# Kernel tuning notes

Hardware: AMD Instinct MI355X
Metric: run time of the kernel (lower is better)

Reference implementation:

```python
import jax, jax.numpy as jnp
import numpy as np

WIN = 3  # win_size from init


def setup_inputs() -> dict:
    key = jax.random.key(0)
    ks = jax.random.split(key, 7)
    B, H, W, d = 8, 128, 128, 128
    N = H * W
    s = d ** -0.5  # param init scale
    return {
        "x": jax.random.normal(ks[0], (B, N, d), dtype=jnp.float32),
        "Wq": jax.random.normal(ks[1], (d, d), dtype=jnp.float32) * s,
        "bq": jax.random.normal(ks[2], (d,), dtype=jnp.float32) * 0.01,
        "Wk": jax.random.normal(ks[3], (d, d), dtype=jnp.float32) * s,
        "bk": jax.random.normal(ks[4], (d,), dtype=jnp.float32) * 0.01,
        "Wv": jax.random.normal(ks[5], (d, d), dtype=jnp.float32) * s,
        "bv": jax.random.normal(ks[6], (d,), dtype=jnp.float32) * 0.01,
        "H": H,
        "W": W,
    }


def reference(x, Wq, bq, Wk, bk, Wv, bv, H, W):
    B, N, d = x.shape
    scale = d ** -0.5
    pad = WIN // 2

    q = (x @ Wq + bq).reshape(B, H, W, d)
    k = (x @ Wk + bk).reshape(B, H, W, d)
    v = (x @ Wv + bv).reshape(B, H, W, d)

    # zero-pad spatial dims (matches F.pad); padded neighbors get logit 0, not -inf
    k_pad = jnp.pad(k, ((0, 0), (pad, pad), (pad, pad), (0, 0)))
    v_pad = jnp.pad(v, ((0, 0), (pad, pad), (pad, pad), (0, 0)))

    scores_l, vs_l = [], []
    for dy in range(WIN):
        for dx in range(WIN):
            k_slice = k_pad[:, dy:dy + H, dx:dx + W]   # [B,H,W,d]
            v_slice = v_pad[:, dy:dy + H, dx:dx + W]
            scores_l.append(jnp.einsum("bhwd,bhwd->bhw", q, k_slice) * scale)
            vs_l.append(v_slice)

    scores = jnp.stack(scores_l, axis=-1)            # [B,H,W,9]
    prob = jax.nn.softmax(scores, axis=-1)           # [B,H,W,9]
    v_stk = jnp.stack(vs_l, axis=-1)                 # [B,H,W,d,9]
    out = jnp.einsum("bhwn,bhwdn->bhwd", prob, v_stk)
    return out.reshape(B, N, d)
```

## Files before the change

kernel.cpp:

```cpp
#include <hip/hip_runtime.h>
#include <stdint.h>

#define B_ 8
#define H_ 128
#define W_ 128
#define D_ 128
#define N_ (H_*W_)
#define M_ (B_*N_)

typedef __attribute__((ext_vector_type(8))) short short8;
typedef __attribute__((ext_vector_type(4))) float floatx4;

typedef const __attribute__((address_space(1))) void* gas_t;
typedef __attribute__((address_space(3))) void* las_t;

__device__ inline unsigned short f2bf(float f){
  union { float f; unsigned int i; } c; c.f = f;
  unsigned int x = c.i;
  x += 0x7FFF + ((x >> 16) & 1);
  return (unsigned short)(x >> 16);
}
__device__ inline float bflo(unsigned int u){
  union { unsigned int i; float f; } c; c.i = u << 16; return c.f;
}
__device__ inline float bfhi(unsigned int u){
  union { unsigned int i; float f; } c; c.i = u & 0xFFFF0000u; return c.f;
}

__global__ void wtrans_kernel(const float* __restrict__ Wq, const float* __restrict__ Wk,
                              const float* __restrict__ Wv, unsigned short* __restrict__ Wt){
  const float* src = blockIdx.x == 0 ? Wq : (blockIdx.x == 1 ? Wk : Wv);
  unsigned short* dst = Wt + blockIdx.x * (D_*D_);
  const int i = blockIdx.y * 256 + threadIdx.x;
  const int k = i >> 7, n = i & 127;
  dst[n*D_ + k] = f2bf(src[i]);
}

__global__ __launch_bounds__(256, 2) void qkv_gemm_kernel(
    const float* __restrict__ x, const unsigned short* __restrict__ Wt,
    const float* __restrict__ bq, const float* __restrict__ bk, const float* __restrict__ bv,
    unsigned short* __restrict__ Q, unsigned short* __restrict__ K, unsigned short* __restrict__ V)
{
  const int rowTile = blockIdx.x;

  __shared__ unsigned short lds[32768];

  const int t = threadIdx.x;
  const int wave = t >> 6, lane = t & 63;

  {
    const float* xrow = x + (size_t)rowTile * 128 * D_;
    #pragma unroll
    for (int p = 0; p < 8; ++p){
      int s = p*256 + t;
      int r = s >> 4, cp = s & 15, c = cp ^ (r & 7);
      const float* gp = xrow + r*D_ + c*8;
      float4 f0 = *(const float4*)gp;
      float4 f1 = *(const float4*)(gp + 4);
      uint4 pk;
      pk.x = (unsigned)f2bf(f0.x) | ((unsigned)f2bf(f0.y) << 16);
      pk.y = (unsigned)f2bf(f0.z) | ((unsigned)f2bf(f0.w) << 16);
      pk.z = (unsigned)f2bf(f1.x) | ((unsigned)f2bf(f1.y) << 16);
      pk.w = (unsigned)f2bf(f1.z) | ((unsigned)f2bf(f1.w) << 16);
      *(uint4*)&lds[s*8] = pk;
    }
  }

  const int wm = (wave >> 1) * 64, wn = (wave & 1) * 64;
  const int m0 = lane & 15, quad = lane >> 4;

  #pragma unroll
  for (int which = 0; which < 3; ++which){
    const float* bias = which == 0 ? bq : (which == 1 ? bk : bv);
    unsigned short* Out = which == 0 ? Q : (which == 1 ? K : V);
    const unsigned short* Wsel = Wt + which * (D_*D_);

    #pragma unroll
    for (int p = 0; p < 8; ++p){
      int s = p*256 + t;
      int n = s >> 4, cp = s & 15, c = cp ^ (n & 7);
      const unsigned short* gp = Wsel + n*128 + c*8;
      unsigned short* lp = (unsigned short*)lds + 16384 + p*2048 + wave*512;
      __builtin_amdgcn_global_load_lds((gas_t)(const void*)gp, (las_t)(void*)lp, 16, 0, 0);
    }
    __syncthreads();

    floatx4 acc[4][4] = {};
    #pragma unroll
    for (int kk = 0; kk < 4; ++kk){
      short8 a[4], b[4];
      #pragma unroll
      for (int i = 0; i < 4; ++i){
        int row = wm + i*16 + m0;
        int c = (kk*4 + quad) ^ (row & 7);
        a[i] = *(const short8*)&lds[row*128 + c*8];
      }
      #pragma unroll
      for (int j = 0; j < 4; ++j){
        int n = wn + j*16 + m0;
        int c = (kk*4 + quad) ^ (n & 7);
        b[j] = *(const short8*)&lds[16384 + n*128 + c*8];
      }
      #pragma unroll
      for (int i = 0; i < 4; ++i)
        #pragma unroll
        for (int j = 0; j < 4; ++j)
          acc[i][j] = __builtin_amdgcn_mfma_f32_16x16x32_bf16(a[i], b[j], acc[i][j], 0, 0, 0);
    }

    __syncthreads();
    unsigned short* Outp = Out + (size_t)rowTile * 128 * D_;
    #pragma unroll
    for (int half = 0; half < 2; ++half){
      if ((wave >> 1) == half){
        #pragma unroll
        for (int j = 0; j < 4; ++j){
          const int col = wn + j*16 + m0;
          const float bb = bias[col];
          #pragma unroll
          for (int i = 0; i < 4; ++i){
            #pragma unroll
            for (int r = 0; r < 4; ++r){
              int lrow = i*16 + quad*4 + r;
              lds[16384 + lrow*136 + col] = f2bf(acc[i][j][r] + bb);
            }
          }
        }
      }
      __syncthreads();
      #pragma unroll
      for (int p = 0; p < 4; ++p){
        int rr = p*16 + (t >> 4), cc = t & 15;
        uint4 vv = *(const uint4*)&lds[16384 + rr*136 + cc*8];
        *(uint4*)(Outp + half*8192 + p*2048 + t*8) = vv;
      }
      __syncthreads();
    }
  }
}

__global__ __launch_bounds__(256, 4) void attn_kernel(
    const unsigned short* __restrict__ Q, const unsigned short* __restrict__ K,
    const unsigned short* __restrict__ V, float* __restrict__ out)
{
  const int t = threadIdx.x;
  const int e16 = t & 15;
  const int pix = blockIdx.x * 16 + (t >> 4);
  const int w = pix & 127;
  const int h = (pix >> 7) & 127;
  const int bbase = pix & ~(N_ - 1);
  const float scale = 0.08838834764831845f;
  const int doff = e16 * 8;
  const size_t off = (size_t)pix * D_ + doff;

  int npix[9]; bool okm[9];
  #pragma unroll
  for (int i = 0; i < 9; ++i){
    const int dy = i/3 - 1, dx = i%3 - 1;
    const int hh = h + dy, ww = w + dx;
    okm[i] = ((unsigned)hh < 128u) && ((unsigned)ww < 128u);
    const int hc = min(max(hh, 0), 127);
    const int wc = min(max(ww, 0), 127);
    npix[i] = bbase + hc*W_ + wc;
  }

  uint4 qu = *(const uint4*)(Q + off);
  uint4 ku[9];
  #pragma unroll
  for (int i = 0; i < 9; ++i)
    ku[i] = *(const uint4*)(K + (size_t)npix[i]*D_ + doff);

  float q[8];
  {
    unsigned uu[4] = {qu.x, qu.y, qu.z, qu.w};
    #pragma unroll
    for (int e = 0; e < 4; ++e){
      q[e*2]     = bflo(uu[e]) * scale;
      q[e*2 + 1] = bfhi(uu[e]) * scale;
    }
  }

  float s[9];
  #pragma unroll
  for (int i = 0; i < 9; ++i){
    unsigned uu[4] = {ku[i].x, ku[i].y, ku[i].z, ku[i].w};
    float acc = 0.f;
    #pragma unroll
    for (int e = 0; e < 4; ++e){
      acc += q[e*2]     * bflo(uu[e]);
      acc += q[e*2 + 1] * bfhi(uu[e]);
    }
    s[i] = okm[i] ? acc : 0.f;
  }

  uint4 vu[9];
  #pragma unroll
  for (int i = 0; i < 9; ++i)
    vu[i] = *(const uint4*)(V + (size_t)npix[i]*D_ + doff);

  #pragma unroll
  for (int i = 0; i < 9; ++i){
    s[i] += __shfl_xor(s[i], 1, 64);
    s[i] += __shfl_xor(s[i], 2, 64);
    s[i] += __shfl_xor(s[i], 4, 64);
    s[i] += __shfl_xor(s[i], 8, 64);
  }

  float m = s[0];
  #pragma unroll
  for (int i = 1; i < 9; ++i) m = fmaxf(m, s[i]);
  float l = 0.f;
  float p[9];
  #pragma unroll
  for (int i = 0; i < 9; ++i){ p[i] = __expf(s[i] - m); l += p[i]; }
  const float inv = 1.f / l;

  float o[8];
  #pragma unroll
  for (int d = 0; d < 8; ++d) o[d] = 0.f;
  #pragma unroll
  for (int i = 0; i < 9; ++i){
    const float pi = okm[i] ? p[i] * inv : 0.f;
    unsigned uu[4] = {vu[i].x, vu[i].y, vu[i].z, vu[i].w};
    #pragma unroll
    for (int e = 0; e < 4; ++e){
      o[e*2]     += pi * bflo(uu[e]);
      o[e*2 + 1] += pi * bfhi(uu[e]);
    }
  }

  float* op = out + off;
  *(float4*)op       = make_float4(o[0], o[1], o[2], o[3]);
  *(float4*)(op + 4) = make_float4(o[4], o[5], o[6], o[7]);
}

extern "C" void kernel_launch(void* const* d_in, const int* in_sizes, int n_in,
                              void* d_out, int out_size, void* d_ws, size_t ws_size,
                              hipStream_t stream)
{
  const float* x  = (const float*)d_in[0];
  const float* Wq = (const float*)d_in[1];
  const float* bq = (const float*)d_in[2];
  const float* Wk = (const float*)d_in[3];
  const float* bk = (const float*)d_in[4];
  const float* Wv = (const float*)d_in[5];
  const float* bv = (const float*)d_in[6];
  float* out = (float*)d_out;

  char* ws = (char*)d_ws;
  unsigned short* Wt = (unsigned short*)ws;
  unsigned short* Q  = (unsigned short*)(ws + (1<<17));
  unsigned short* K  = (unsigned short*)(ws + (1<<17) + (size_t)M_*D_*2);
  unsigned short* V  = (unsigned short*)(ws + (1<<17) + (size_t)2*M_*D_*2);

  hipLaunchKernelGGL(wtrans_kernel, dim3(3, 64), dim3(256), 0, stream, Wq, Wk, Wv, Wt);
  hipLaunchKernelGGL(qkv_gemm_kernel, dim3(M_/128), dim3(256), 0, stream,
                     x, Wt, bq, bk, bv, Q, K, V);
  hipLaunchKernelGGL(attn_kernel, dim3(M_/16), dim3(256), 0, stream, Q, K, V, out);
}
```

Baseline: 184.8 us.

## Retile QKV GEMM into 64-row by 32-column blocks with register-resident x fragments

The QKV projection GEMM now splits its output columns into four 32-wide groups across blockIdx.x and uses 64-row tiles, raising the block count and allowing 4 blocks per CU. Each wave loads its x fragment straight from global memory into MFMA registers, converts it to bf16 there, and skips the LDS staging of x. Only the 32-column weight slices for Q, K and V go through LDS. The epilogue no longer transposes through LDS: operands are swapped in the MFMA and each lane writes packed bf16 directly. In exchange, x is fetched by four blocks instead of one, which leans on cache reuse, and the output stores are narrower and less coalesced.

```diff
diff --git a/kernel.cpp b/kernel.cpp
--- a/kernel.cpp
+++ b/kernel.cpp
@@ -36,105 +36,78 @@
   dst[n*D_ + k] = f2bf(src[i]);
 }
 
-__global__ __launch_bounds__(256, 2) void qkv_gemm_kernel(
+__global__ __launch_bounds__(256, 4) void qkv_gemm_kernel(
     const float* __restrict__ x, const unsigned short* __restrict__ Wt,
     const float* __restrict__ bq, const float* __restrict__ bk, const float* __restrict__ bv,
     unsigned short* __restrict__ Q, unsigned short* __restrict__ K, unsigned short* __restrict__ V)
 {
-  const int rowTile = blockIdx.x;
-
-  __shared__ unsigned short lds[32768];
+  const int cg = blockIdx.x;
+  const int rowTile = blockIdx.y;
+
+  __shared__ unsigned short lds[12288];
 
   const int t = threadIdx.x;
   const int wave = t >> 6, lane = t & 63;
-
+  const int m0 = lane & 15, quad = lane >> 4;
+
+  #pragma unroll
+  for (int which = 0; which < 3; ++which){
+    const unsigned short* Wsel = Wt + which*(D_*D_) + cg*32*D_;
+    #pragma unroll
+    for (int p = 0; p < 2; ++p){
+      int s = p*256 + t;
+      int n = s >> 4, cp = s & 15, c = cp ^ (n & 7);
+      __builtin_amdgcn_global_load_lds((gas_t)(const void*)(Wsel + n*128 + c*8),
+          (las_t)(void*)((unsigned short*)lds + which*4096 + p*2048 + wave*512), 16, 0, 0);
+    }
+  }
+
+  short8 a[4];
   {
-    const float* xrow = x + (size_t)rowTile * 128 * D_;
-    #pragma unroll
-    for (int p = 0; p < 8; ++p){
-      int s = p*256 + t;
-      int r = s >> 4, cp = s & 15, c = cp ^ (r & 7);
-      const float* gp = xrow + r*D_ + c*8;
-      float4 f0 = *(const float4*)gp;
-      float4 f1 = *(const float4*)(gp + 4);
-      uint4 pk;
-      pk.x = (unsigned)f2bf(f0.x) | ((unsigned)f2bf(f0.y) << 16);
-      pk.y = (unsigned)f2bf(f0.z) | ((unsigned)f2bf(f0.w) << 16);
-      pk.z = (unsigned)f2bf(f1.x) | ((unsigned)f2bf(f1.y) << 16);
-      pk.w = (unsigned)f2bf(f1.z) | ((unsigned)f2bf(f1.w) << 16);
-      *(uint4*)&lds[s*8] = pk;
-    }
-  }
-
-  const int wm = (wave >> 1) * 64, wn = (wave & 1) * 64;
-  const int m0 = lane & 15, quad = lane >> 4;
-
+    const float* xrow = x + (size_t)(rowTile*64 + wave*16 + m0) * D_ + quad*8;
+    float4 f[4][2];
+    #pragma unroll
+    for (int kk = 0; kk < 4; ++kk){
+      f[kk][0] = *(const float4*)(xrow + kk*32);
+      f[kk][1] = *(const float4*)(xrow + kk*32 + 4);
+    }
+    __builtin_amdgcn_sched_barrier(0);
+    #pragma unroll
+    for (int kk = 0; kk < 4; ++kk){
+      short8 v;
+      v[0] = (short)f2bf(f[kk][0].x); v[1] = (short)f2bf(f[kk][0].y);
+      v[2] = (short)f2bf(f[kk][0].z); v[3] = (short)f2bf(f[kk][0].w);
+      v[4] = (short)f2bf(f[kk][1].x); v[5] = (short)f2bf(f[kk][1].y);
+      v[6] = (short)f2bf(f[kk][1].z); v[7] = (short)f2bf(f[kk][1].w);
+      a[kk] = v;
+    }
+  }
+  __syncthreads();
+
+  const int row = rowTile*64 + wave*16 + m0;
   #pragma unroll
   for (int which = 0; which < 3; ++which){
+    floatx4 acc[2] = {};
+    #pragma unroll
+    for (int kk = 0; kk < 4; ++kk){
+      #pragma unroll
+      for (int j = 0; j < 2; ++j){
+        int n = j*16 + m0;
+        int c = (kk*4 + quad) ^ (n & 7);
+        short8 b = *(const short8*)&lds[which*4096 + n*128 + c*8];
+        acc[j] = __builtin_amdgcn_mfma_f32_16x16x32_bf16(b, a[kk], acc[j], 0, 0, 0);
+      }
+    }
     const float* bias = which == 0 ? bq : (which == 1 ? bk : bv);
     unsigned short* Out = which == 0 ? Q : (which == 1 ? K : V);
-    const unsigned short* Wsel = Wt + which * (D_*D_);
-
-    #pragma unroll
-    for (int p = 0; p < 8; ++p){
-      int s = p*256 + t;
-      int n = s >> 4, cp = s & 15, c = cp ^ (n & 7);
-      const unsigned short* gp = Wsel + n*128 + c*8;
-      unsigned short* lp = (unsigned short*)lds + 16384 + p*2048 + wave*512;
-      __builtin_amdgcn_global_load_lds((gas_t)(const void*)gp, (las_t)(void*)lp, 16, 0, 0);
-    }
-    __syncthreads();
-
-    floatx4 acc[4][4] = {};
-    #pragma unroll
-    for (int kk = 0; kk < 4; ++kk){
-      short8 a[4], b[4];
-      #pragma unroll
-      for (int i = 0; i < 4; ++i){
-        int row = wm + i*16 + m0;
-        int c = (kk*4 + quad) ^ (row & 7);
-        a[i] = *(const short8*)&lds[row*128 + c*8];
-      }
-      #pragma unroll
-      for (int j = 0; j < 4; ++j){
-        int n = wn + j*16 + m0;
-        int c = (kk*4 + quad) ^ (n & 7);
-        b[j] = *(const short8*)&lds[16384 + n*128 + c*8];
-      }
-      #pragma unroll
-      for (int i = 0; i < 4; ++i)
-        #pragma unroll
-        for (int j = 0; j < 4; ++j)
-          acc[i][j] = __builtin_amdgcn_mfma_f32_16x16x32_bf16(a[i], b[j], acc[i][j], 0, 0, 0);
-    }
-
-    __syncthreads();
-    unsigned short* Outp = Out + (size_t)rowTile * 128 * D_;
-    #pragma unroll
-    for (int half = 0; half < 2; ++half){
-      if ((wave >> 1) == half){
-        #pragma unroll
-        for (int j = 0; j < 4; ++j){
-          const int col = wn + j*16 + m0;
-          const float bb = bias[col];
-          #pragma unroll
-          for (int i = 0; i < 4; ++i){
-            #pragma unroll
-            for (int r = 0; r < 4; ++r){
-              int lrow = i*16 + quad*4 + r;
-              lds[16384 + lrow*136 + col] = f2bf(acc[i][j][r] + bb);
-            }
-          }
-        }
-      }
-      __syncthreads();
-      #pragma unroll
-      for (int p = 0; p < 4; ++p){
-        int rr = p*16 + (t >> 4), cc = t & 15;
-        uint4 vv = *(const uint4*)&lds[16384 + rr*136 + cc*8];
-        *(uint4*)(Outp + half*8192 + p*2048 + t*8) = vv;
-      }
-      __syncthreads();
+    #pragma unroll
+    for (int j = 0; j < 2; ++j){
+      const int col = cg*32 + j*16 + quad*4;
+      const float4 bb = *(const float4*)&bias[col];
+      uint2 pk;
+      pk.x = (unsigned)f2bf(acc[j][0] + bb.x) | ((unsigned)f2bf(acc[j][1] + bb.y) << 16);
+      pk.y = (unsigned)f2bf(acc[j][2] + bb.z) | ((unsigned)f2bf(acc[j][3] + bb.w) << 16);
+      *(uint2*)(Out + (size_t)row * D_ + col) = pk;
     }
   }
 }
@@ -254,7 +227,7 @@
   unsigned short* V  = (unsigned short*)(ws + (1<<17) + (size_t)2*M_*D_*2);
 
   hipLaunchKernelGGL(wtrans_kernel, dim3(3, 64), dim3(256), 0, stream, Wq, Wk, Wv, Wt);
-  hipLaunchKernelGGL(qkv_gemm_kernel, dim3(M_/128), dim3(256), 0, stream,
+  hipLaunchKernelGGL(qkv_gemm_kernel, dim3(4, M_/64), dim3(256), 0, stream,
                      x, Wt, bq, bk, bv, Q, K, V);
   hipLaunchKernelGGL(attn_kernel, dim3(M_/16), dim3(256), 0, stream, Q, K, V, out);
 }
```

Measured after the change: 215.0 us. +16.4%, slower.
